# Kernel optimization log

Measured on AMD Instinct MI355X. Metric: run time of the kernel, lower is better.

Reference implementation:

```python
import jax, jax.numpy as jnp
import numpy as np

BS, NN = 4096, 16          # batch size, robots per sample
OBS_PN, ACT_PN = 10, 2     # per-node obs / action dims
HID = 128                  # hidden_dim; hidden_depth = 2
N = BS * NN                # total nodes


def _build_edges():
    # complete graph per sample including self-loops (PyG GCNConv adds self-loops;
    # self-loop weight exp(-0)=1 matches PyG fill_value=1.0)
    s = np.repeat(np.arange(NN), NN)
    d = np.tile(np.arange(NN), NN)
    off = np.repeat(np.arange(BS) * NN, NN * NN)
    src = np.tile(s, BS) + off
    dst = np.tile(d, BS) + off
    return jnp.asarray(src, jnp.int32), jnp.asarray(dst, jnp.int32)


def setup_inputs() -> dict:
    key = jax.random.key(0)
    ks = jax.random.split(key, 16)
    inp = {
        "obs": jax.random.normal(ks[0], (BS, NN * OBS_PN), jnp.float32),
        "action": jax.random.normal(ks[1], (BS, NN * ACT_PN), jnp.float32),
    }
    dims = [(OBS_PN, HID), (HID, HID), (HID, 1)]  # trunk_input_size = 10
    i = 2
    for q in ("Q1", "Q2"):
        for l, (din, dout) in enumerate(dims):
            inp[f"{q}_W{l}"] = jax.random.normal(ks[i], (din, dout), jnp.float32) / np.sqrt(din).astype(np.float32)
            inp[f"{q}_b{l}"] = jnp.zeros((dout,), jnp.float32)
            i += 1
    inp["src"], inp["dst"] = _build_edges()
    return inp


def _gcn(x, W, b, src, dst, norm):
    # GCNConv: out = scatter_add(norm * (x @ W)[src] -> dst) + b
    y = x @ W                                  # [N, F_out]
    msg = norm[:, None] * y[src]               # [E, F_out]
    return jax.ops.segment_sum(msg, dst, num_segments=N) + b


def reference(obs, action, Q1_W0, Q1_b0, Q1_W1, Q1_b1, Q1_W2, Q1_b2,
              Q2_W0, Q2_b0, Q2_W1, Q2_b1, Q2_W2, Q2_b2, src, dst):
    feat = jnp.concatenate(
        [obs.reshape(N, OBS_PN), action.reshape(N, ACT_PN)], axis=-1)  # [N, 12]
    loc = feat[:, :2]          # robot_loc
    x = feat[:, ACT_PN:]       # input_features[:, gnn_action_dim:] -> [N, 10]

    # per-edge distance weights + symmetric GCN normalization
    w = jnp.exp(-jnp.linalg.norm(loc[dst] - loc[src], axis=-1))        # [E]
    deg = jax.ops.segment_sum(w, dst, num_segments=N)                  # [N]
    dinv = jnp.where(deg > 0, deg, 1.0) ** -0.5
    norm = dinv[src] * w * dinv[dst]

    def net(W0, b0, W1, b1, W2, b2):
        h = jax.nn.relu(_gcn(x, W0, b0, src, dst, norm))
        h = jax.nn.relu(_gcn(h, W1, b1, src, dst, norm))
        return _gcn(h, W2, b2, src, dst, norm).reshape(BS, NN)

    q1 = net(Q1_W0, Q1_b0, Q1_W1, Q1_b1, Q1_W2, Q1_b2)
    q2 = net(Q2_W0, Q2_b0, Q2_W1, Q2_b1, Q2_W2, Q2_b2)
    return (q1, q2)
```

## Files before the change

kernel.cpp:

```cpp
#include <hip/hip_runtime.h>


typedef short    s16x8 __attribute__((ext_vector_type(8)));
typedef float    f32x4 __attribute__((ext_vector_type(4)));
typedef unsigned u32x4 __attribute__((ext_vector_type(4)));

#define MFMA32(a, b, c) __builtin_amdgcn_mfma_f32_16x16x32_bf16((a), (b), (c), 0, 0, 0)

constexpr int WS_W0F = 0;
constexpr int WS_W1H = 8192;
constexpr int WS_W1L = 40960;

__device__ __forceinline__ unsigned short bf16_rn(float f) {
  unsigned u = __float_as_uint(f);
  u = u + 0x7FFFu + ((u >> 16) & 1u);
  return (unsigned short)(u >> 16);
}
__device__ __forceinline__ void split2(float f, unsigned short& h, unsigned short& l) {
  h = bf16_rn(f);
  float fh = __uint_as_float(((unsigned)h) << 16);
  l = bf16_rn(f - fh);
}
__device__ __forceinline__ void split_pk(float f0, float f1,
                                         unsigned& H, unsigned& L) {
  unsigned u0 = __float_as_uint(f0) + 0x8000u;
  unsigned u1 = __float_as_uint(f1) + 0x8000u;
  H = __builtin_amdgcn_perm(u1, u0, 0x07060302u);
  float r0 = f0 - __uint_as_float(u0 & 0xFFFF0000u);
  float r1 = f1 - __uint_as_float(u1 & 0xFFFF0000u);
  L = __builtin_amdgcn_perm(__float_as_uint(r1), __float_as_uint(r0), 0x07060302u);
}
__device__ __forceinline__ s16x8 as_s16x8(u32x4 v) {
  return __builtin_bit_cast(s16x8, v);
}

extern "C" __global__ void __launch_bounds__(256)
prep_weights(const float* __restrict__ w0a, const float* __restrict__ w1a,
             const float* __restrict__ w0b, const float* __restrict__ w1b,
             unsigned short* __restrict__ ws) {
  const int tid = threadIdx.x;
  if (blockIdx.x < 16) {
    int f = blockIdx.x * 256 + tid;
    int lane = f & 63, t = (f >> 6) & 7, q = (f >> 9) & 3, net = f >> 11;
    const float* W1 = net ? w1b : w1a;
    int c = 16 * t + (lane & 15);
    int kbase = 32 * q + 4 * (lane >> 4);
    s16x8 vh, vl;
#pragma unroll
    for (int e = 0; e < 8; ++e) {
      int k = kbase + (e & 3) + 16 * (e >> 2);
      unsigned short h, l; split2(W1[k * 128 + c], h, l);
      vh[e] = (short)h; vl[e] = (short)l;
    }
    int base = ((net * 4 + q) * 8 + t) * 64 + lane;
    ((s16x8*)(ws + WS_W1H))[base] = vh;
    ((s16x8*)(ws + WS_W1L))[base] = vl;
  } else {
#pragma unroll
    for (int i = 0; i < 4; ++i) {
      int f = i * 256 + tid;
      int lane = f & 63, t = (f >> 6) & 7, net = (f >> 9) & 1;
      const float* W0 = net ? w0b : w0a;
      int c = 16 * t + (lane & 15);
      int kbase = 4 * (lane >> 4);
      s16x8 v;
#pragma unroll
      for (int j = 0; j < 4; ++j) {
        int k = kbase + j;
        float w = (k < 10) ? W0[k * 128 + c] : 0.f;
        unsigned short h, l; split2(w, h, l);
        v[j] = (short)h; v[4 + j] = (short)l;
      }
      ((s16x8*)(ws + WS_W0F))[(net * 8 + t) * 64 + lane] = v;
    }
  }
}

extern "C" __global__ void __launch_bounds__(256, 4)
gcnn_critic_kernel(const float* __restrict__ obs, const float* __restrict__ act,
                   const float* __restrict__ b0a, const float* __restrict__ b1a,
                   const float* __restrict__ w2a, const float* __restrict__ b2a,
                   const float* __restrict__ b0b, const float* __restrict__ b1b,
                   const float* __restrict__ w2b, const float* __restrict__ b2b,
                   const unsigned short* __restrict__ ws,
                   float* __restrict__ out) {
  __shared__ float RAW[4][200];
  const int tid  = threadIdx.x;
  const int lane = tid & 63;
  const int wv   = tid >> 6;
  const int l15  = lane & 15;
  const int lg   = lane >> 4;
  const int batch = blockIdx.x * 4 + wv;

  float* raw = RAW[wv];

#pragma unroll
  for (int i = 0; i < 3; ++i) {
    int j = i * 64 + lane;
    if (j < 192) {
      float v = (j < 160) ? obs[batch * 160 + j] : act[batch * 32 + (j - 160)];
      raw[j] = v;
    }
  }
  __syncthreads();

  float wreg[4];
  float wsum = 0.f;
#pragma unroll
  for (int j = 0; j < 4; ++j) {
    int s = 4 * lg + j;
    float dx = raw[l15 * 10]     - raw[s * 10];
    float dy = raw[l15 * 10 + 1] - raw[s * 10 + 1];
    float w = expf(-sqrtf(dx * dx + dy * dy));
    wreg[j] = w;
    wsum += w;
  }
  wsum += __shfl_xor(wsum, 16, 64);
  wsum += __shfl_xor(wsum, 32, 64);
  float dv = 1.0f / sqrtf(wsum);
  float Af[4];
#pragma unroll
  for (int j = 0; j < 4; ++j) {
    float dvs = __shfl(dv, 4 * lg + j, 64);
    Af[j] = wreg[j] * dv * dvs;
  }
  unsigned AH01, AL01, AH23, AL23;
  split_pk(Af[0], Af[1], AH01, AL01);
  split_pk(Af[2], Af[3], AH23, AL23);
  const s16x8 ABh = as_s16x8((u32x4){AH01, AH23, AH01, AH23});
  const s16x8 ABl = as_s16x8((u32x4){AL01, AL23, 0u, 0u});

  float xv[4];
#pragma unroll
  for (int j = 0; j < 4; ++j) {
    int s = 4 * lg + j;
    float v = 0.f;
    if (l15 < 8)       v = raw[s * 10 + 2 + l15];
    else if (l15 < 10) v = raw[160 + s * 2 + (l15 - 8)];
    xv[j] = v;
  }
  unsigned xH0, xL0, xH1, xL1;
  split_pk(xv[0], xv[1], xH0, xL0);
  split_pk(xv[2], xv[3], xH1, xL1);
  const s16x8 xop = as_s16x8((u32x4){xH0, xH1, xL0, xL1});

  f32x4 z0 = {0.f, 0.f, 0.f, 0.f};
  z0 = MFMA32(xop, ABh, z0);
  z0 = MFMA32(xop, ABl, z0);
  unsigned zH0, zL0, zH1, zL1;
  split_pk(z0[0], z0[1], zH0, zL0);
  split_pk(z0[2], z0[3], zH1, zL1);
  const s16x8 z0op = as_s16x8((u32x4){zH0, zH1, zL0, zL1});

  const s16x8* W0F = (const s16x8*)(ws + WS_W0F);
  const s16x8* W1H = (const s16x8*)(ws + WS_W1H);
  const s16x8* W1L = (const s16x8*)(ws + WS_W1L);
  const s16x8 zero8 = {0, 0, 0, 0, 0, 0, 0, 0};

#pragma unroll 1
  for (int qsel = 0; qsel < 2; ++qsel) {
    const float* B0 = qsel ? b0b : b0a;
    const float* B1 = qsel ? b1b : b1a;
    const float* W2 = qsel ? w2b : w2a;
    const float b2v = qsel ? b2b[0] : b2a[0];
    const int net = qsel;

    s16x8 h1op[8];
#pragma unroll
    for (int t = 0; t < 8; ++t) {
      s16x8 wf = W0F[(net * 8 + t) * 64 + lane];
      s16x8 Bh = __builtin_shufflevector(wf, wf, 0, 1, 2, 3, 0, 1, 2, 3);
      s16x8 Bl = __builtin_shufflevector(wf, zero8, 4, 5, 6, 7, 8, 9, 10, 11);
      float bv = B0[16 * t + l15];
      f32x4 a = {0.f, 0.f, 0.f, 0.f};
      a = MFMA32(z0op, Bh, a);
      a = MFMA32(z0op, Bl, a);
      float a0 = fmaxf(a[0] + bv, 0.f), a1 = fmaxf(a[1] + bv, 0.f);
      float a2 = fmaxf(a[2] + bv, 0.f), a3 = fmaxf(a[3] + bv, 0.f);
      unsigned H0, L0, H1, L1;
      split_pk(a0, a1, H0, L0);
      split_pk(a2, a3, H1, L1);
      h1op[t] = as_s16x8((u32x4){H0, H1, L0, L1});
    }

    unsigned zHw[8][2], zLw[8][2];
#pragma unroll
    for (int t = 0; t < 8; ++t) {
      f32x4 z = {0.f, 0.f, 0.f, 0.f};
      z = MFMA32(h1op[t], ABh, z);
      z = MFMA32(h1op[t], ABl, z);
      split_pk(z[0], z[1], zHw[t][0], zLw[t][0]);
      split_pk(z[2], z[3], zHw[t][1], zLw[t][1]);
    }

    f32x4 acc[8];
#pragma unroll
    for (int t = 0; t < 8; ++t) acc[t] = (f32x4){0.f, 0.f, 0.f, 0.f};
    __builtin_amdgcn_s_setprio(1);
#pragma unroll
    for (int q = 0; q < 4; ++q) {
      s16x8 zh8 = as_s16x8(
          (u32x4){zHw[2 * q][0], zHw[2 * q][1], zHw[2 * q + 1][0], zHw[2 * q + 1][1]});
      s16x8 zl8 = as_s16x8(
          (u32x4){zLw[2 * q][0], zLw[2 * q][1], zLw[2 * q + 1][0], zLw[2 * q + 1][1]});
      int base = ((net * 4 + q) * 8) * 64 + lane;
#pragma unroll
      for (int t = 0; t < 8; ++t) {
        s16x8 Wh = W1H[base + t * 64];
        s16x8 Wl = W1L[base + t * 64];
        acc[t] = MFMA32(zh8, Wh, acc[t]);
        acc[t] = MFMA32(zh8, Wl, acc[t]);
        acc[t] = MFMA32(zl8, Wh, acc[t]);
      }
    }
    __builtin_amdgcn_s_setprio(0);

    float part[4] = {0.f, 0.f, 0.f, 0.f};
#pragma unroll
    for (int t = 0; t < 8; ++t) {
      float bv  = B1[16 * t + l15];
      float wv2 = W2[16 * t + l15];
#pragma unroll
      for (int r = 0; r < 4; ++r)
        part[r] += fmaxf(acc[t][r] + bv, 0.f) * wv2;
    }
#pragma unroll
    for (int d = 1; d < 16; d <<= 1)
#pragma unroll
      for (int r = 0; r < 4; ++r)
        part[r] += __shfl_xor(part[r], d, 64);
    float pq = Af[0] * part[0] + Af[1] * part[1] + Af[2] * part[2] + Af[3] * part[3];
    pq += __shfl_xor(pq, 16, 64);
    pq += __shfl_xor(pq, 32, 64);
    if (lane < 16)
      out[qsel * 65536 + batch * 16 + l15] = pq + b2v;
  }
}

extern "C" void kernel_launch(void* const* d_in, const int* in_sizes, int n_in,
                              void* d_out, int out_size, void* d_ws, size_t ws_size,
                              hipStream_t stream) {
  (void)in_sizes; (void)n_in; (void)out_size; (void)ws_size;
  const float* obs = (const float*)d_in[0];
  const float* act = (const float*)d_in[1];
  const float* w0a = (const float*)d_in[2];
  const float* b0a = (const float*)d_in[3];
  const float* w1a = (const float*)d_in[4];
  const float* b1a = (const float*)d_in[5];
  const float* w2a = (const float*)d_in[6];
  const float* b2a = (const float*)d_in[7];
  const float* w0b = (const float*)d_in[8];
  const float* b0b = (const float*)d_in[9];
  const float* w1b = (const float*)d_in[10];
  const float* b1b = (const float*)d_in[11];
  const float* w2b = (const float*)d_in[12];
  const float* b2b = (const float*)d_in[13];
  unsigned short* ws = (unsigned short*)d_ws;

  prep_weights<<<17, 256, 0, stream>>>(w0a, w1a, w0b, w1b, ws);
  gcnn_critic_kernel<<<1024, 256, 0, stream>>>(
      obs, act, b0a, b1a, w2a, b2a, b0b, b1b, w2b, b2b, ws, (float*)d_out);
}
```

Measured before the change: 116.0 us.

## Stage W1 weights in LDS per block and split the two Q-nets across blocks

Each block now handles eight batches for a single Q-network, chosen by block parity, using 512 threads. The block's hi/lo bf16 W1 fragments (64 KB) are copied into dynamic shared memory so the inner MFMA loop reads operands from LDS instead of global/L1. Before, every wave loaded both networks' W1 fragments straight from global memory. The change aims to cut repeated global and L1 weight traffic and shorten each wave's serial work. In exchange, about 70 KB of LDS per block limits resident blocks per CU, and the prologue that loads the graph and raw inputs now runs twice, once per network.

Result: faster. 108.5 us (-6.4%).

```diff
diff --git a/kernel.cpp b/kernel.cpp
--- a/kernel.cpp
+++ b/kernel.cpp
@@ -10,6 +10,9 @@
 constexpr int WS_W0F = 0;
 constexpr int WS_W1H = 8192;
 constexpr int WS_W1L = 40960;
+
+constexpr int LDS_RAW   = 65536;
+constexpr int SMEM_TOTAL = 65536 + 8 * 200 * 4;
 
 __device__ __forceinline__ unsigned short bf16_rn(float f) {
   unsigned u = __float_as_uint(f);
@@ -76,7 +79,7 @@
   }
 }
 
-extern "C" __global__ void __launch_bounds__(256, 4)
+extern "C" __global__ void __launch_bounds__(512, 4)
 gcnn_critic_kernel(const float* __restrict__ obs, const float* __restrict__ act,
                    const float* __restrict__ b0a, const float* __restrict__ b1a,
                    const float* __restrict__ w2a, const float* __restrict__ b2a,
@@ -84,16 +87,27 @@
                    const float* __restrict__ w2b, const float* __restrict__ b2b,
                    const unsigned short* __restrict__ ws,
                    float* __restrict__ out) {
-  __shared__ float RAW[4][200];
+  extern __shared__ char smem[];
   const int tid  = threadIdx.x;
   const int lane = tid & 63;
   const int wv   = tid >> 6;
   const int l15  = lane & 15;
   const int lg   = lane >> 4;
-  const int batch = blockIdx.x * 4 + wv;
-
-  float* raw = RAW[wv];
-
+  const int net  = blockIdx.x & 1;
+  const int batch = (blockIdx.x >> 1) * 8 + wv;
+
+  s16x8* lH = (s16x8*)smem;
+  s16x8* lL = (s16x8*)(smem + 32768);
+  float* raw = (float*)(smem + LDS_RAW) + wv * 200;
+
+  {
+    const s16x8* gH = (const s16x8*)(ws + WS_W1H) + net * 2048;
+    const s16x8* gL = (const s16x8*)(ws + WS_W1L) + net * 2048;
+#pragma unroll
+    for (int k = 0; k < 4; ++k) lH[tid + k * 512] = gH[tid + k * 512];
+#pragma unroll
+    for (int k = 0; k < 4; ++k) lL[tid + k * 512] = gL[tid + k * 512];
+  }
 #pragma unroll
   for (int i = 0; i < 3; ++i) {
     int j = i * 64 + lane;
@@ -153,88 +167,81 @@
   const s16x8 z0op = as_s16x8((u32x4){zH0, zH1, zL0, zL1});
 
   const s16x8* W0F = (const s16x8*)(ws + WS_W0F);
-  const s16x8* W1H = (const s16x8*)(ws + WS_W1H);
-  const s16x8* W1L = (const s16x8*)(ws + WS_W1L);
+  const float* B0 = net ? b0b : b0a;
+  const float* B1 = net ? b1b : b1a;
+  const float* W2 = net ? w2b : w2a;
+  const float b2v = net ? b2b[0] : b2a[0];
   const s16x8 zero8 = {0, 0, 0, 0, 0, 0, 0, 0};
 
-#pragma unroll 1
-  for (int qsel = 0; qsel < 2; ++qsel) {
-    const float* B0 = qsel ? b0b : b0a;
-    const float* B1 = qsel ? b1b : b1a;
-    const float* W2 = qsel ? w2b : w2a;
-    const float b2v = qsel ? b2b[0] : b2a[0];
-    const int net = qsel;
-
-    s16x8 h1op[8];
+  s16x8 h1op[8];
+#pragma unroll
+  for (int t = 0; t < 8; ++t) {
+    s16x8 wf = W0F[(net * 8 + t) * 64 + lane];
+    s16x8 Bh = __builtin_shufflevector(wf, wf, 0, 1, 2, 3, 0, 1, 2, 3);
+    s16x8 Bl = __builtin_shufflevector(wf, zero8, 4, 5, 6, 7, 8, 9, 10, 11);
+    float bv = B0[16 * t + l15];
+    f32x4 a = {0.f, 0.f, 0.f, 0.f};
+    a = MFMA32(z0op, Bh, a);
+    a = MFMA32(z0op, Bl, a);
+    float a0 = fmaxf(a[0] + bv, 0.f), a1 = fmaxf(a[1] + bv, 0.f);
+    float a2 = fmaxf(a[2] + bv, 0.f), a3 = fmaxf(a[3] + bv, 0.f);
+    unsigned H0, L0, H1, L1;
+    split_pk(a0, a1, H0, L0);
+    split_pk(a2, a3, H1, L1);
+    h1op[t] = as_s16x8((u32x4){H0, H1, L0, L1});
+  }
+
+  unsigned zHw[8][2], zLw[8][2];
+#pragma unroll
+  for (int t = 0; t < 8; ++t) {
+    f32x4 z = {0.f, 0.f, 0.f, 0.f};
+    z = MFMA32(h1op[t], ABh, z);
+    z = MFMA32(h1op[t], ABl, z);
+    split_pk(z[0], z[1], zHw[t][0], zLw[t][0]);
+    split_pk(z[2], z[3], zHw[t][1], zLw[t][1]);
+  }
+
+  f32x4 acc[8];
+#pragma unroll
+  for (int t = 0; t < 8; ++t) acc[t] = (f32x4){0.f, 0.f, 0.f, 0.f};
+  __builtin_amdgcn_s_setprio(1);
+#pragma unroll
+  for (int q = 0; q < 4; ++q) {
+    s16x8 zh8 = as_s16x8(
+        (u32x4){zHw[2 * q][0], zHw[2 * q][1], zHw[2 * q + 1][0], zHw[2 * q + 1][1]});
+    s16x8 zl8 = as_s16x8(
+        (u32x4){zLw[2 * q][0], zLw[2 * q][1], zLw[2 * q + 1][0], zLw[2 * q + 1][1]});
+    int base = (q * 8) * 64 + lane;
 #pragma unroll
     for (int t = 0; t < 8; ++t) {
-      s16x8 wf = W0F[(net * 8 + t) * 64 + lane];
-      s16x8 Bh = __builtin_shufflevector(wf, wf, 0, 1, 2, 3, 0, 1, 2, 3);
-      s16x8 Bl = __builtin_shufflevector(wf, zero8, 4, 5, 6, 7, 8, 9, 10, 11);
-      float bv = B0[16 * t + l15];
-      f32x4 a = {0.f, 0.f, 0.f, 0.f};
-      a = MFMA32(z0op, Bh, a);
-      a = MFMA32(z0op, Bl, a);
-      float a0 = fmaxf(a[0] + bv, 0.f), a1 = fmaxf(a[1] + bv, 0.f);
-      float a2 = fmaxf(a[2] + bv, 0.f), a3 = fmaxf(a[3] + bv, 0.f);
-      unsigned H0, L0, H1, L1;
-      split_pk(a0, a1, H0, L0);
-      split_pk(a2, a3, H1, L1);
-      h1op[t] = as_s16x8((u32x4){H0, H1, L0, L1});
-    }
-
-    unsigned zHw[8][2], zLw[8][2];
-#pragma unroll
-    for (int t = 0; t < 8; ++t) {
-      f32x4 z = {0.f, 0.f, 0.f, 0.f};
-      z = MFMA32(h1op[t], ABh, z);
-      z = MFMA32(h1op[t], ABl, z);
-      split_pk(z[0], z[1], zHw[t][0], zLw[t][0]);
-      split_pk(z[2], z[3], zHw[t][1], zLw[t][1]);
-    }
-
-    f32x4 acc[8];
-#pragma unroll
-    for (int t = 0; t < 8; ++t) acc[t] = (f32x4){0.f, 0.f, 0.f, 0.f};
-    __builtin_amdgcn_s_setprio(1);
-#pragma unroll
-    for (int q = 0; q < 4; ++q) {
-      s16x8 zh8 = as_s16x8(
-          (u32x4){zHw[2 * q][0], zHw[2 * q][1], zHw[2 * q + 1][0], zHw[2 * q + 1][1]});
-      s16x8 zl8 = as_s16x8(
-          (u32x4){zLw[2 * q][0], zLw[2 * q][1], zLw[2 * q + 1][0], zLw[2 * q + 1][1]});
-      int base = ((net * 4 + q) * 8) * 64 + lane;
-#pragma unroll
-      for (int t = 0; t < 8; ++t) {
-        s16x8 Wh = W1H[base + t * 64];
-        s16x8 Wl = W1L[base + t * 64];
-        acc[t] = MFMA32(zh8, Wh, acc[t]);
-        acc[t] = MFMA32(zh8, Wl, acc[t]);
-        acc[t] = MFMA32(zl8, Wh, acc[t]);
-      }
-    }
-    __builtin_amdgcn_s_setprio(0);
-
-    float part[4] = {0.f, 0.f, 0.f, 0.f};
-#pragma unroll
-    for (int t = 0; t < 8; ++t) {
-      float bv  = B1[16 * t + l15];
-      float wv2 = W2[16 * t + l15];
-#pragma unroll
-      for (int r = 0; r < 4; ++r)
-        part[r] += fmaxf(acc[t][r] + bv, 0.f) * wv2;
-    }
-#pragma unroll
-    for (int d = 1; d < 16; d <<= 1)
-#pragma unroll
-      for (int r = 0; r < 4; ++r)
-        part[r] += __shfl_xor(part[r], d, 64);
-    float pq = Af[0] * part[0] + Af[1] * part[1] + Af[2] * part[2] + Af[3] * part[3];
-    pq += __shfl_xor(pq, 16, 64);
-    pq += __shfl_xor(pq, 32, 64);
-    if (lane < 16)
-      out[qsel * 65536 + batch * 16 + l15] = pq + b2v;
-  }
+      s16x8 Wh = lH[base + t * 64];
+      s16x8 Wl = lL[base + t * 64];
+      acc[t] = MFMA32(zh8, Wh, acc[t]);
+      acc[t] = MFMA32(zh8, Wl, acc[t]);
+      acc[t] = MFMA32(zl8, Wh, acc[t]);
+    }
+  }
+  __builtin_amdgcn_s_setprio(0);
+
+  float part[4] = {0.f, 0.f, 0.f, 0.f};
+#pragma unroll
+  for (int t = 0; t < 8; ++t) {
+    float bv  = B1[16 * t + l15];
+    float wv2 = W2[16 * t + l15];
+#pragma unroll
+    for (int r = 0; r < 4; ++r)
+      part[r] += fmaxf(acc[t][r] + bv, 0.f) * wv2;
+  }
+#pragma unroll
+  for (int d = 1; d < 16; d <<= 1)
+#pragma unroll
+    for (int r = 0; r < 4; ++r)
+      part[r] += __shfl_xor(part[r], d, 64);
+  float pq = Af[0] * part[0] + Af[1] * part[1] + Af[2] * part[2] + Af[3] * part[3];
+  pq += __shfl_xor(pq, 16, 64);
+  pq += __shfl_xor(pq, 32, 64);
+  if (lane < 16)
+    out[net * 65536 + batch * 16 + l15] = pq + b2v;
 }
 
 extern "C" void kernel_launch(void* const* d_in, const int* in_sizes, int n_in,
@@ -258,6 +265,6 @@
   unsigned short* ws = (unsigned short*)d_ws;
 
   prep_weights<<<17, 256, 0, stream>>>(w0a, w1a, w0b, w1b, ws);
-  gcnn_critic_kernel<<<1024, 256, 0, stream>>>(
+  gcnn_critic_kernel<<<1024, 512, SMEM_TOTAL, stream>>>(
       obs, act, b0a, b1a, w2a, b2a, b0b, b1b, w2b, b2b, ws, (float*)d_out);
 }
```
